# Kernel optimization log

Hardware: AMD Instinct MI355X
Metric: run time of the kernel (lower is better)

Reference implementation:

```python
import jax, jax.numpy as jnp
import numpy as np

D_MODEL = 1024
NUM_HEADS = 16
HEAD_DIM = D_MODEL // NUM_HEADS


def setup_inputs() -> dict:
    key = jax.random.key(0)
    ks = jax.random.split(key, 11)
    B, N = 2, 2048
    s = 1.0 / np.sqrt(D_MODEL)
    return {
        "query": jax.random.normal(ks[0], (B, N, D_MODEL), jnp.float32),
        "key":   jax.random.normal(ks[1], (B, N, D_MODEL), jnp.float32),
        "value": jax.random.normal(ks[2], (B, N, D_MODEL), jnp.float32),
        "Wq": jax.random.normal(ks[3], (D_MODEL, D_MODEL), jnp.float32) * s,
        "bq": jax.random.normal(ks[4], (D_MODEL,), jnp.float32) * 0.01,
        "Wk": jax.random.normal(ks[5], (D_MODEL, D_MODEL), jnp.float32) * s,
        "bk": jax.random.normal(ks[6], (D_MODEL,), jnp.float32) * 0.01,
        "Wv": jax.random.normal(ks[7], (D_MODEL, D_MODEL), jnp.float32) * s,
        "bv": jax.random.normal(ks[8], (D_MODEL,), jnp.float32) * 0.01,
        "Wo": jax.random.normal(ks[9], (D_MODEL, D_MODEL), jnp.float32) * s,
        "bo": jax.random.normal(ks[10], (D_MODEL,), jnp.float32) * 0.01,
    }


def _split_heads(x):
    # [B, N, d_model] -> [B, H, N, head_dim]
    B, N, _ = x.shape
    return x.reshape(B, N, NUM_HEADS, HEAD_DIM).transpose(0, 2, 1, 3)


def reference(query, key, value, Wq, bq, Wk, bk, Wv, bv, Wo, bo):
    B, N, _ = query.shape
    q = _split_heads(query @ Wq.T + bq)  # [B,H,N,dh]
    k = _split_heads(key @ Wk.T + bk)
    v = _split_heads(value @ Wv.T + bv)
    # NOTE: faithful to source: no 1/sqrt(head_dim) scaling.
    scores = jnp.einsum("bhnd,bhmd->bhnm", q, k)
    attn = jax.nn.softmax(scores, axis=-1)
    out = jnp.einsum("bhnm,bhmd->bhnd", attn, v)
    out = out.transpose(0, 2, 1, 3).reshape(B, N, D_MODEL)
    return out @ Wo.T + bo
```

## Files before the change

kernel.cpp:

```cpp
#include <hip/hip_runtime.h>
#include <cstdint>

#define DEV __device__ __forceinline__

typedef __bf16 bf16x8 __attribute__((ext_vector_type(8)));
typedef short s16x8 __attribute__((ext_vector_type(8)));
typedef float f32x4 __attribute__((ext_vector_type(4)));
typedef unsigned short u16;

constexpr int D_MODEL = 1024;
constexpr int SEQ = 2048;
constexpr float LOG2E = 1.4426950408889634f;
constexpr float SHIFT = 64.0f;

DEV u16 f2bf(float f) {
  uint32_t u = __float_as_uint(f);
  u += 0x7fff + ((u >> 16) & 1);
  return (u16)(u >> 16);
}

DEV void load_lds16(const void* g, void* l) {
  __builtin_amdgcn_global_load_lds((const __attribute__((address_space(1))) void*)g,
                                   (__attribute__((address_space(3))) void*)l, 16, 0, 0);
}

struct ConvArgs {
  const float* src[7];
  u16* dst[7];
  int n[7];
};

__global__ __launch_bounds__(256) void convert_kernel(ConvArgs a) {
  const int t = blockIdx.y;
  const int i = (blockIdx.x * 256 + threadIdx.x) * 4;
  if (i >= a.n[t]) return;
  const float4 v = *(const float4*)(a.src[t] + i);
  ushort4 o;
  o.x = f2bf(v.x); o.y = f2bf(v.y); o.z = f2bf(v.z); o.w = f2bf(v.w);
  *(ushort4*)(a.dst[t] + i) = o;
}

struct GemmArgs {
  const u16* A[3];
  const u16* W[3];
  const float* bias[3];
  u16* out[3];
  float scale[3];
};

__global__ __launch_bounds__(256, 2) void gemm_qkv(GemmArgs args) {
  __shared__ u16 lds[2][2][128 * 64];
  const int bid = blockIdx.x;
  const int xcd = bid & 7, j = bid >> 3;
  const int z = j >> 5;
  const int r0 = j & 31;
  const int m0 = (xcd * 4 + (r0 >> 3)) * 128;
  const int n0 = (r0 & 7) * 128;
  const u16* __restrict__ A = args.A[z];
  const u16* __restrict__ W = args.W[z];
  const int tid = threadIdx.x;
  const int lane = tid & 63, wid = tid >> 6;
  const int quad = lane >> 4, l16 = lane & 15;
  const int wm = wid >> 1, wn = wid & 1;

  f32x4 acc[4][4] = {};

#define GSTAGE(T, B)                                                              \
  {                                                                               \
    _Pragma("unroll")                                                             \
    for (int p = 0; p < 4; ++p) {                                                 \
      int c = p * 256 + tid;                                                      \
      int row = c >> 3;                                                           \
      int g = ((c & 7) ^ (row & 7)) * 8;                                          \
      load_lds16(A + (size_t)(m0 + row) * D_MODEL + (T) * 64 + g, &lds[B][0][c * 8]); \
      load_lds16(W + (size_t)(n0 + row) * D_MODEL + (T) * 64 + g, &lds[B][1][c * 8]); \
    }                                                                             \
  }

  GSTAGE(0, 0);
  __syncthreads();

  for (int kt = 0; kt < 16; ++kt) {
    if (kt + 1 < 16) GSTAGE(kt + 1, (kt + 1) & 1);
    const u16* lA = lds[kt & 1][0];
    const u16* lB = lds[kt & 1][1];
#pragma unroll
    for (int ks = 0; ks < 2; ++ks) {
      bf16x8 af[4], bfr[4];
#pragma unroll
      for (int mt = 0; mt < 4; ++mt) {
        int r = wm * 64 + mt * 16 + l16;
        int ch = (ks * 4 + quad) ^ (r & 7);
        af[mt] = *(const bf16x8*)&lA[r * 64 + ch * 8];
      }
#pragma unroll
      for (int nt = 0; nt < 4; ++nt) {
        int r = wn * 64 + nt * 16 + l16;
        int ch = (ks * 4 + quad) ^ (r & 7);
        bfr[nt] = *(const bf16x8*)&lB[r * 64 + ch * 8];
      }
#pragma unroll
      for (int mt = 0; mt < 4; ++mt)
#pragma unroll
        for (int nt = 0; nt < 4; ++nt)
          acc[mt][nt] = __builtin_amdgcn_mfma_f32_16x16x32_bf16(af[mt], bfr[nt], acc[mt][nt], 0, 0, 0);
    }
    __syncthreads();
  }
#undef GSTAGE

  const float* __restrict__ bias = args.bias[z];
  u16* out = args.out[z];
  float sc = args.scale[z];
  if (z == 2) {
#pragma unroll
    for (int nt = 0; nt < 4; ++nt) {
      int col = n0 + wn * 64 + nt * 16 + l16;
      float bv = bias[col];
      int h = col >> 6, d = col & 63;
#pragma unroll
      for (int mt = 0; mt < 4; ++mt) {
        int mb = m0 + wm * 64 + mt * 16 + quad * 4;
        int b = mb >> 11, tt = mb & 2047;
        ushort4 o;
        o.x = f2bf(acc[mt][nt][0] + bv);
        o.y = f2bf(acc[mt][nt][1] + bv);
        o.z = f2bf(acc[mt][nt][2] + bv);
        o.w = f2bf(acc[mt][nt][3] + bv);
        *(ushort4*)(out + ((size_t)(b * 16 + h) * 64 + d) * SEQ + tt) = o;
      }
    }
  } else {
#pragma unroll
    for (int nt = 0; nt < 4; ++nt) {
      int col = n0 + wn * 64 + nt * 16 + l16;
      float bv = bias[col];
      int h = col >> 6, d = col & 63;
#pragma unroll
      for (int mt = 0; mt < 4; ++mt) {
        int mb = m0 + wm * 64 + mt * 16 + quad * 4;
#pragma unroll
        for (int r = 0; r < 4; ++r) {
          int tok = mb + r;
          int b = tok >> 11, tt = tok & 2047;
          out[(((size_t)(b * 16 + h) * SEQ + tt) << 6) + d] = f2bf((acc[mt][nt][r] + bv) * sc);
        }
      }
    }
  }
}

__global__ __launch_bounds__(256, 2) void gemm_out(const u16* __restrict__ A,
                                                   const u16* __restrict__ W,
                                                   const float* __restrict__ bias,
                                                   float* __restrict__ out) {
  __shared__ u16 lds[2][(128 + 64) * 64];
  const int bid = blockIdx.x;
  const int xcd = bid & 7, j = bid >> 3;
  const int m0 = (xcd * 4 + (j >> 4)) * 128;
  const int n0 = (j & 15) * 64;
  const int tid = threadIdx.x;
  const int lane = tid & 63, wid = tid >> 6;
  const int quad = lane >> 4, l16 = lane & 15;
  const int wm = wid >> 1, wn = wid & 1;

  f32x4 acc[4][2] = {};

#define OSTAGE(T, B)                                                              \
  {                                                                               \
    _Pragma("unroll")                                                             \
    for (int p = 0; p < 4; ++p) {                                                 \
      int c = p * 256 + tid;                                                      \
      int row = c >> 3;                                                           \
      int g = ((c & 7) ^ (row & 7)) * 8;                                          \
      load_lds16(A + (size_t)(m0 + row) * D_MODEL + (T) * 64 + g, &lds[B][c * 8]); \
    }                                                                             \
    _Pragma("unroll")                                                             \
    for (int p = 0; p < 2; ++p) {                                                 \
      int c = p * 256 + tid;                                                      \
      int row = c >> 3;                                                           \
      int g = ((c & 7) ^ (row & 7)) * 8;                                          \
      load_lds16(W + (size_t)(n0 + row) * D_MODEL + (T) * 64 + g,                 \
                 &lds[B][128 * 64 + c * 8]);                                      \
    }                                                                             \
  }

  OSTAGE(0, 0);
  __syncthreads();

  for (int kt = 0; kt < 16; ++kt) {
    if (kt + 1 < 16) OSTAGE(kt + 1, (kt + 1) & 1);
    const u16* lA = lds[kt & 1];
    const u16* lW = lds[kt & 1] + 128 * 64;
#pragma unroll
    for (int ks = 0; ks < 2; ++ks) {
      bf16x8 af[4], wf[2];
#pragma unroll
      for (int mt = 0; mt < 4; ++mt) {
        int r = wm * 64 + mt * 16 + l16;
        int ch = (ks * 4 + quad) ^ (r & 7);
        af[mt] = *(const bf16x8*)&lA[r * 64 + ch * 8];
      }
#pragma unroll
      for (int nt = 0; nt < 2; ++nt) {
        int r = wn * 32 + nt * 16 + l16;
        int ch = (ks * 4 + quad) ^ (r & 7);
        wf[nt] = *(const bf16x8*)&lW[r * 64 + ch * 8];
      }
#pragma unroll
      for (int mt = 0; mt < 4; ++mt)
#pragma unroll
        for (int nt = 0; nt < 2; ++nt)
          acc[mt][nt] = __builtin_amdgcn_mfma_f32_16x16x32_bf16(af[mt], wf[nt], acc[mt][nt], 0, 0, 0);
    }
    __syncthreads();
  }
#undef OSTAGE

#pragma unroll
  for (int nt = 0; nt < 2; ++nt) {
    int col = n0 + wn * 32 + nt * 16 + l16;
    float bv = bias[col];
#pragma unroll
    for (int mt = 0; mt < 4; ++mt) {
      int mb = m0 + wm * 64 + mt * 16 + quad * 4;
#pragma unroll
      for (int r = 0; r < 4; ++r)
        out[(size_t)(mb + r) * D_MODEL + col] = acc[mt][nt][r] + bv;
    }
  }
}

__global__ __launch_bounds__(512, 4) void attn_kernel(const u16* __restrict__ Q,
                                                      const u16* __restrict__ K,
                                                      const u16* __restrict__ Vt,
                                                      u16* __restrict__ O) {
  __shared__ u16 sm[3][2][64 * 64];
  const int bid = blockIdx.x;
  const int xcd = bid & 7, jj = bid >> 3;
  const int bh = xcd + 8 * (jj >> 4);
  const int q0 = (jj & 15) * 128;
  const int tid = threadIdx.x;
  const int lane = tid & 63, w = tid >> 6;
  const int quad = lane >> 4, l16 = lane & 15;
  const int kb = w & 1;
  const int pair = w >> 1;

  const u16* kbase = K + (size_t)bh * SEQ * 64;
  const u16* vtbase = Vt + (size_t)bh * 64 * SEQ;

  bf16x8 qf[2][2];
#pragma unroll
  for (int qh = 0; qh < 2; ++qh) {
    const u16* qrow = Q + ((size_t)bh * SEQ + q0 + pair * 32 + qh * 16 + l16) * 64;
    qf[qh][0] = *(const bf16x8*)(qrow + quad * 8);
    qf[qh][1] = *(const bf16x8*)(qrow + 32 + quad * 8);
  }

  bf16x8 onesA;
  {
    __bf16 v = (l16 == 0) ? (__bf16)1.0f : (__bf16)0.0f;
#pragma unroll
    for (int j = 0; j < 8; ++j) onesA[j] = v;
  }

  f32x4 acc[2][5] = {};
  const f32x4 minit = {-SHIFT, -SHIFT, -SHIFT, -SHIFT};

#define STAGE(T, B)                                                               \
  {                                                                               \
    int c = tid;                                                                  \
    int row = c >> 3;                                                             \
    int km = (row & 32) | (((row >> 2) & 3) << 3) | (((row >> 4) & 1) << 2) |     \
             (row & 3);                                                           \
    int g = ((c & 7) ^ (row & 7)) * 8;                                            \
    load_lds16(kbase + (size_t)((T) * 64 + km) * 64 + g, &sm[B][0][c * 8]);       \
    load_lds16(vtbase + (size_t)row * SEQ + (T) * 64 + g, &sm[B][1][c * 8]);      \
  }

  STAGE(0, 0);
  STAGE(1, 1);
  asm volatile("s_waitcnt vmcnt(2)" ::: "memory");
  __builtin_amdgcn_s_barrier();
  __builtin_amdgcn_sched_barrier(0);

  for (int t = 0; t < SEQ / 64; ++t) {
    if (t + 2 < SEQ / 64) STAGE(t + 2, (t + 2) % 3);
    const u16* lK = sm[t % 3][0];
    const u16* lV = sm[t % 3][1];

    bf16x8 kf[2][2];
#pragma unroll
    for (int nt = 0; nt < 2; ++nt) {
      int r = kb * 32 + nt * 16 + l16;
#pragma unroll
      for (int ks = 0; ks < 2; ++ks) {
        int ch = (ks * 4 + quad) ^ (r & 7);
        kf[nt][ks] = *(const bf16x8*)&lK[r * 64 + ch * 8];
      }
    }

    s16x8 pf[2];
#pragma unroll
    for (int qh = 0; qh < 2; ++qh) {
      f32x4 s0 = __builtin_amdgcn_mfma_f32_16x16x32_bf16(kf[0][0], qf[qh][0], minit, 0, 0, 0);
      s0 = __builtin_amdgcn_mfma_f32_16x16x32_bf16(kf[0][1], qf[qh][1], s0, 0, 0, 0);
      f32x4 s1 = __builtin_amdgcn_mfma_f32_16x16x32_bf16(kf[1][0], qf[qh][0], minit, 0, 0, 0);
      s1 = __builtin_amdgcn_mfma_f32_16x16x32_bf16(kf[1][1], qf[qh][1], s1, 0, 0, 0);
      bf16x8 pb;
#pragma unroll
      for (int r = 0; r < 4; ++r) {
        pb[r] = (__bf16)__builtin_amdgcn_exp2f(s0[r]);
        pb[4 + r] = (__bf16)__builtin_amdgcn_exp2f(s1[r]);
      }
      pf[qh] = __builtin_bit_cast(s16x8, pb);
    }

#pragma unroll
    for (int dt = 0; dt < 4; ++dt) {
      int row = dt * 16 + l16;
      int ch = (kb * 4 + quad) ^ (row & 7);
      bf16x8 vf = *(const bf16x8*)&lV[row * 64 + ch * 8];
#pragma unroll
      for (int qh = 0; qh < 2; ++qh)
        acc[qh][dt] = __builtin_amdgcn_mfma_f32_16x16x32_bf16(
            vf, __builtin_bit_cast(bf16x8, pf[qh]), acc[qh][dt], 0, 0, 0);
    }
#pragma unroll
    for (int qh = 0; qh < 2; ++qh)
      acc[qh][4] = __builtin_amdgcn_mfma_f32_16x16x32_bf16(
          onesA, __builtin_bit_cast(bf16x8, pf[qh]), acc[qh][4], 0, 0, 0);

    if (t < SEQ / 64 - 2) {
      asm volatile("s_waitcnt vmcnt(2)" ::: "memory");
      __builtin_amdgcn_s_barrier();
      __builtin_amdgcn_sched_barrier(0);
    } else if (t == SEQ / 64 - 2) {
      asm volatile("s_waitcnt vmcnt(0)" ::: "memory");
      __builtin_amdgcn_s_barrier();
      __builtin_amdgcn_sched_barrier(0);
    }
  }
#undef STAGE

  __syncthreads();

  float* red = (float*)&sm[0][0][0];
  if (kb == 1) {
#pragma unroll
    for (int qh = 0; qh < 2; ++qh)
#pragma unroll
      for (int dt = 0; dt < 5; ++dt)
        *(f32x4*)&red[(((pair * 2 + qh) * 5 + dt) * 64 + lane) * 4] = acc[qh][dt];
  }
  __syncthreads();
  if (kb == 0) {
    const int b = bh >> 4, h = bh & 15;
#pragma unroll
    for (int qh = 0; qh < 2; ++qh) {
#pragma unroll
      for (int dt = 0; dt < 5; ++dt)
        acc[qh][dt] += *(const f32x4*)&red[(((pair * 2 + qh) * 5 + dt) * 64 + lane) * 4];
      float sum = __shfl(acc[qh][4][0], l16, 64);
      float inv = 1.0f / sum;
      const int tok = b * SEQ + q0 + pair * 32 + qh * 16 + l16;
      u16* obase = O + (size_t)tok * D_MODEL + h * 64;
#pragma unroll
      for (int dt = 0; dt < 4; ++dt) {
        ushort4 o;
        o.x = f2bf(acc[qh][dt][0] * inv);
        o.y = f2bf(acc[qh][dt][1] * inv);
        o.z = f2bf(acc[qh][dt][2] * inv);
        o.w = f2bf(acc[qh][dt][3] * inv);
        *(ushort4*)(obase + dt * 16 + quad * 4) = o;
      }
    }
  }
}

extern "C" void kernel_launch(void* const* d_in, const int* in_sizes, int n_in,
                              void* d_out, int out_size, void* d_ws, size_t ws_size,
                              hipStream_t stream) {
  const float* q  = (const float*)d_in[0];
  const float* k  = (const float*)d_in[1];
  const float* v  = (const float*)d_in[2];
  const float* Wq = (const float*)d_in[3];
  const float* bq = (const float*)d_in[4];
  const float* Wk = (const float*)d_in[5];
  const float* bk = (const float*)d_in[6];
  const float* Wv = (const float*)d_in[7];
  const float* bv = (const float*)d_in[8];
  const float* Wo = (const float*)d_in[9];
  const float* bo = (const float*)d_in[10];

  uint8_t* ws = (uint8_t*)d_ws;
  const size_t MB = 1024 * 1024;
  u16* Xq  = (u16*)(ws + 0 * MB);
  u16* Xk  = (u16*)(ws + 8 * MB);
  u16* Xv  = (u16*)(ws + 16 * MB);
  u16* Wqb = (u16*)(ws + 24 * MB);
  u16* Wkb = (u16*)(ws + 26 * MB);
  u16* Wvb = (u16*)(ws + 28 * MB);
  u16* Wob = (u16*)(ws + 30 * MB);
  u16* Qb  = (u16*)(ws + 32 * MB);
  u16* Kb  = (u16*)(ws + 40 * MB);
  u16* Vtb = (u16*)(ws + 48 * MB);
  u16* Ob  = Xq;

  ConvArgs ca;
  ca.src[0] = q;  ca.dst[0] = Xq;  ca.n[0] = 4194304;
  ca.src[1] = k;  ca.dst[1] = Xk;  ca.n[1] = 4194304;
  ca.src[2] = v;  ca.dst[2] = Xv;  ca.n[2] = 4194304;
  ca.src[3] = Wq; ca.dst[3] = Wqb; ca.n[3] = 1048576;
  ca.src[4] = Wk; ca.dst[4] = Wkb; ca.n[4] = 1048576;
  ca.src[5] = Wv; ca.dst[5] = Wvb; ca.n[5] = 1048576;
  ca.src[6] = Wo; ca.dst[6] = Wob; ca.n[6] = 1048576;
  convert_kernel<<<dim3(4096, 7), 256, 0, stream>>>(ca);

  GemmArgs ga;
  ga.A[0] = Xq; ga.A[1] = Xk; ga.A[2] = Xv;
  ga.W[0] = Wqb; ga.W[1] = Wkb; ga.W[2] = Wvb;
  ga.bias[0] = bq; ga.bias[1] = bk; ga.bias[2] = bv;
  ga.out[0] = Qb; ga.out[1] = Kb; ga.out[2] = Vtb;
  ga.scale[0] = LOG2E; ga.scale[1] = 1.0f; ga.scale[2] = 1.0f;
  gemm_qkv<<<dim3(768), 256, 0, stream>>>(ga);

  attn_kernel<<<dim3(512), 512, 0, stream>>>(Qb, Kb, Vtb, Ob);

  gemm_out<<<dim3(512), 256, 0, stream>>>(Ob, Wob, bo, (float*)d_out);
}
```

Measured before the change: 199.0 us.

## Deepen attention K/V pipeline to four stages, add MFMA priority, compact convert grid

The attention kernel's LDS ring grows from three to four K/V buffers, so tiles are prefetched three iterations ahead and the vmcnt waits are adjusted to match. QK and PV MFMA groups are batched and wrapped in s_setprio, with the V fragment loads hoisted ahead of the PV MFMAs. Separately, the convert kernel's 2D grid, where most weight-conversion blocks exited early, becomes a dense 1D grid of exactly the needed blocks. The extra LDS buffer raises shared memory per block from 48KB to 64KB, which may limit occupancy.

```diff
diff --git a/kernel.cpp b/kernel.cpp
--- a/kernel.cpp
+++ b/kernel.cpp
@@ -27,13 +27,14 @@
 struct ConvArgs {
   const float* src[7];
   u16* dst[7];
-  int n[7];
 };
 
 __global__ __launch_bounds__(256) void convert_kernel(ConvArgs a) {
-  const int t = blockIdx.y;
-  const int i = (blockIdx.x * 256 + threadIdx.x) * 4;
-  if (i >= a.n[t]) return;
+  const int bid = blockIdx.x;
+  int t, base;
+  if (bid < 12288) { t = bid >> 12; base = (bid & 4095) << 10; }
+  else { int r = bid - 12288; t = 3 + (r >> 10); base = (r & 1023) << 10; }
+  const int i = base + threadIdx.x * 4;
   const float4 v = *(const float4*)(a.src[t] + i);
   ushort4 o;
   o.x = f2bf(v.x); o.y = f2bf(v.y); o.z = f2bf(v.z); o.w = f2bf(v.w);
@@ -235,7 +236,7 @@
                                                       const u16* __restrict__ K,
                                                       const u16* __restrict__ Vt,
                                                       u16* __restrict__ O) {
-  __shared__ u16 sm[3][2][64 * 64];
+  __shared__ u16 sm[4][2][64 * 64];
   const int bid = blockIdx.x;
   const int xcd = bid & 7, jj = bid >> 3;
   const int bh = xcd + 8 * (jj >> 4);
@@ -280,14 +281,15 @@
 
   STAGE(0, 0);
   STAGE(1, 1);
-  asm volatile("s_waitcnt vmcnt(2)" ::: "memory");
+  STAGE(2, 2);
+  asm volatile("s_waitcnt vmcnt(4)" ::: "memory");
   __builtin_amdgcn_s_barrier();
   __builtin_amdgcn_sched_barrier(0);
 
   for (int t = 0; t < SEQ / 64; ++t) {
-    if (t + 2 < SEQ / 64) STAGE(t + 2, (t + 2) % 3);
-    const u16* lK = sm[t % 3][0];
-    const u16* lV = sm[t % 3][1];
+    if (t + 3 < SEQ / 64) STAGE(t + 3, (t + 3) & 3);
+    const u16* lK = sm[t & 3][0];
+    const u16* lV = sm[t & 3][1];
 
     bf16x8 kf[2][2];
 #pragma unroll
@@ -300,38 +302,54 @@
       }
     }
 
+    f32x4 s[2][2];
+    __builtin_amdgcn_s_setprio(1);
+#pragma unroll
+    for (int qh = 0; qh < 2; ++qh) {
+      s[qh][0] = __builtin_amdgcn_mfma_f32_16x16x32_bf16(kf[0][0], qf[qh][0], minit, 0, 0, 0);
+      s[qh][0] = __builtin_amdgcn_mfma_f32_16x16x32_bf16(kf[0][1], qf[qh][1], s[qh][0], 0, 0, 0);
+      s[qh][1] = __builtin_amdgcn_mfma_f32_16x16x32_bf16(kf[1][0], qf[qh][0], minit, 0, 0, 0);
+      s[qh][1] = __builtin_amdgcn_mfma_f32_16x16x32_bf16(kf[1][1], qf[qh][1], s[qh][1], 0, 0, 0);
+    }
+    __builtin_amdgcn_s_setprio(0);
+
     s16x8 pf[2];
 #pragma unroll
     for (int qh = 0; qh < 2; ++qh) {
-      f32x4 s0 = __builtin_amdgcn_mfma_f32_16x16x32_bf16(kf[0][0], qf[qh][0], minit, 0, 0, 0);
-      s0 = __builtin_amdgcn_mfma_f32_16x16x32_bf16(kf[0][1], qf[qh][1], s0, 0, 0, 0);
-      f32x4 s1 = __builtin_amdgcn_mfma_f32_16x16x32_bf16(kf[1][0], qf[qh][0], minit, 0, 0, 0);
-      s1 = __builtin_amdgcn_mfma_f32_16x16x32_bf16(kf[1][1], qf[qh][1], s1, 0, 0, 0);
       bf16x8 pb;
 #pragma unroll
       for (int r = 0; r < 4; ++r) {
-        pb[r] = (__bf16)__builtin_amdgcn_exp2f(s0[r]);
-        pb[4 + r] = (__bf16)__builtin_amdgcn_exp2f(s1[r]);
+        pb[r] = (__bf16)__builtin_amdgcn_exp2f(s[qh][0][r]);
+        pb[4 + r] = (__bf16)__builtin_amdgcn_exp2f(s[qh][1][r]);
       }
       pf[qh] = __builtin_bit_cast(s16x8, pb);
     }
 
+    bf16x8 vf[4];
 #pragma unroll
     for (int dt = 0; dt < 4; ++dt) {
       int row = dt * 16 + l16;
       int ch = (kb * 4 + quad) ^ (row & 7);
-      bf16x8 vf = *(const bf16x8*)&lV[row * 64 + ch * 8];
+      vf[dt] = *(const bf16x8*)&lV[row * 64 + ch * 8];
+    }
+    __builtin_amdgcn_s_setprio(1);
+#pragma unroll
+    for (int dt = 0; dt < 4; ++dt)
 #pragma unroll
       for (int qh = 0; qh < 2; ++qh)
         acc[qh][dt] = __builtin_amdgcn_mfma_f32_16x16x32_bf16(
-            vf, __builtin_bit_cast(bf16x8, pf[qh]), acc[qh][dt], 0, 0, 0);
-    }
+            vf[dt], __builtin_bit_cast(bf16x8, pf[qh]), acc[qh][dt], 0, 0, 0);
 #pragma unroll
     for (int qh = 0; qh < 2; ++qh)
       acc[qh][4] = __builtin_amdgcn_mfma_f32_16x16x32_bf16(
           onesA, __builtin_bit_cast(bf16x8, pf[qh]), acc[qh][4], 0, 0, 0);
-
-    if (t < SEQ / 64 - 2) {
+    __builtin_amdgcn_s_setprio(0);
+
+    if (t <= SEQ / 64 - 4) {
+      asm volatile("s_waitcnt vmcnt(4)" ::: "memory");
+      __builtin_amdgcn_s_barrier();
+      __builtin_amdgcn_sched_barrier(0);
+    } else if (t == SEQ / 64 - 3) {
       asm volatile("s_waitcnt vmcnt(2)" ::: "memory");
       __builtin_amdgcn_s_barrier();
       __builtin_amdgcn_sched_barrier(0);
@@ -408,14 +426,14 @@
   u16* Ob  = Xq;
 
   ConvArgs ca;
-  ca.src[0] = q;  ca.dst[0] = Xq;  ca.n[0] = 4194304;
-  ca.src[1] = k;  ca.dst[1] = Xk;  ca.n[1] = 4194304;
-  ca.src[2] = v;  ca.dst[2] = Xv;  ca.n[2] = 4194304;
-  ca.src[3] = Wq; ca.dst[3] = Wqb; ca.n[3] = 1048576;
-  ca.src[4] = Wk; ca.dst[4] = Wkb; ca.n[4] = 1048576;
-  ca.src[5] = Wv; ca.dst[5] = Wvb; ca.n[5] = 1048576;
-  ca.src[6] = Wo; ca.dst[6] = Wob; ca.n[6] = 1048576;
-  convert_kernel<<<dim3(4096, 7), 256, 0, stream>>>(ca);
+  ca.src[0] = q;  ca.dst[0] = Xq;
+  ca.src[1] = k;  ca.dst[1] = Xk;
+  ca.src[2] = v;  ca.dst[2] = Xv;
+  ca.src[3] = Wq; ca.dst[3] = Wqb;
+  ca.src[4] = Wk; ca.dst[4] = Wkb;
+  ca.src[5] = Wv; ca.dst[5] = Wvb;
+  ca.src[6] = Wo; ca.dst[6] = Wob;
+  convert_kernel<<<dim3(16384), 256, 0, stream>>>(ca);
 
   GemmArgs ga;
   ga.A[0] = Xq; ga.A[1] = Xk; ga.A[2] = Xv;
```

Measured after the change: 204.8 us. +2.9%, slower.
